# Kernel optimization log

Hardware: AMD Instinct MI355X
Metric: run time of the kernel (lower is better)

## Reference

```python
import jax, jax.numpy as jnp
import numpy as np

N = 400_000
B = 64          # number of segments (point clouds)
IN_C = 128
INTER = (256, 512, 512)
OUT_C = 512


def setup_inputs() -> dict:
    key = jax.random.key(0)
    ks = jax.random.split(key, 12)
    pos_emd = jax.random.normal(ks[0], (N, IN_C), dtype=jnp.float32)
    radius_p_batch = jnp.sort(jax.random.randint(ks[1], (N,), 0, B))

    def lin(k, fin, fout):
        kw, kb = jax.random.split(k)
        s = 1.0 / np.sqrt(fin)
        W = jax.random.uniform(kw, (fin, fout), jnp.float32, -s, s)
        b = jax.random.uniform(kb, (fout,), jnp.float32, -s, s)
        return W, b

    W1, b1 = lin(ks[2], IN_C, INTER[0])
    W2, b2 = lin(ks[3], INTER[0], INTER[1])
    W3, b3 = lin(ks[4], INTER[1], INTER[2])
    W4, b4 = lin(ks[5], IN_C + INTER[2], OUT_C)
    W5, b5 = lin(ks[6], OUT_C, OUT_C)
    return {
        "pos_emd": pos_emd, "radius_p_batch": radius_p_batch,
        "W1": W1, "b1": b1, "W2": W2, "b2": b2, "W3": W3, "b3": b3,
        "W4": W4, "b4": b4, "W5": W5, "b5": b5,
    }


def reference(pos_emd, radius_p_batch, W1, b1, W2, b2, W3, b3, W4, b4, W5, b5):
    # mlp1: Linear-ReLU-Linear-ReLU-Linear
    h = jax.nn.relu(pos_emd @ W1 + b1)
    h = jax.nn.relu(h @ W2 + b2)
    h = h @ W3 + b3                              # [N, 512]
    # global max pool over segments
    g = jax.ops.segment_max(h, radius_p_batch, num_segments=B)  # [B, 512]
    # broadcast each segment's global feature back to its points (ids sorted)
    g_rep = g[radius_p_batch]                    # [N, 512]
    z = jnp.concatenate((pos_emd, g_rep), axis=-1)  # [N, 640]
    # mlp2: Linear-ReLU-Linear
    z = jax.nn.relu(z @ W4 + b4)
    z = z @ W5 + b5                              # [N, 512]
    return jax.ops.segment_max(z, radius_p_batch, num_segments=B)  # [B, 512]
```

## Files before the change

### kernel.cpp

```cpp
#include <hip/hip_runtime.h>
#include <stdint.h>


typedef __bf16 bf16;
typedef __bf16 bf16x4 __attribute__((ext_vector_type(4)));
typedef __bf16 bf16x8 __attribute__((ext_vector_type(8)));
typedef float f32x4 __attribute__((ext_vector_type(4)));
typedef __attribute__((address_space(3))) char lds_char;

#define N_PTS 400000
#define ORD_NEG_INF 0x007FFFFFu

__device__ __forceinline__ unsigned f2ord(float f) {
  unsigned u = __float_as_uint(f);
  return (u & 0x80000000u) ? ~u : (u | 0x80000000u);
}
__device__ __forceinline__ float ord2f(unsigned o) {
  unsigned u = (o & 0x80000000u) ? (o ^ 0x80000000u) : ~o;
  return __uint_as_float(u);
}

__device__ __forceinline__ void gld16(const bf16* g, lds_char* l) {
  __builtin_amdgcn_global_load_lds((const __attribute__((address_space(1))) void*)g,
                                   (__attribute__((address_space(3))) void*)l, 16, 0, 0);
}

#define DSR(dst, preg, IMM) \
  asm volatile("ds_read_b128 %0, %1 offset:%c2" : "=&v"(dst) : "v"(preg), "n"(IMM))

#define SCHED0 __builtin_amdgcn_sched_barrier(0)
#define LGKM0 do { asm volatile("s_waitcnt lgkmcnt(0)"); SCHED0; } while (0)
#define SBARR do { __builtin_amdgcn_s_barrier(); SCHED0; } while (0)
#define VMW4 do { asm volatile("s_waitcnt vmcnt(4)"); SCHED0; } while (0)
#define VMW0 do { asm volatile("s_waitcnt vmcnt(0)"); SCHED0; } while (0)

__global__ void k_init(unsigned* g_ord, unsigned* out_u) {
  int i = blockIdx.x * 256 + threadIdx.x;
  if (i < 64 * 512) { g_ord[i] = ORD_NEG_INF; out_u[i] = ORD_NEG_INF; }
}

__global__ void k_convX(const float* __restrict__ x, bf16* __restrict__ y, long n4) {
  long i = (long)blockIdx.x * 256 + threadIdx.x;
  long stride = (long)gridDim.x * 256;
  for (; i < n4; i += stride) {
    float4 v = ((const float4*)x)[i];
    bf16x4 o = {(bf16)v.x, (bf16)v.y, (bf16)v.z, (bf16)v.w};
    ((bf16x4*)y)[i] = o;
  }
}

__global__ void k_convWt(const float* __restrict__ W, bf16* __restrict__ Wt, int K, int Nout) {
  int idx = blockIdx.x * 256 + threadIdx.x;
  if (idx < K * Nout) {
    int k = idx / Nout, c = idx - k * Nout;
    Wt[(size_t)c * K + k] = (bf16)W[idx];
  }
}

__global__ void k_segbias(const unsigned* __restrict__ g_ord, const float* __restrict__ W4,
                          const float* __restrict__ b4, float* __restrict__ sb) {
  const int s = blockIdx.x, c = threadIdx.x;
  __shared__ float gs[512];
  gs[c] = ord2f(g_ord[s * 512 + c]);
  __syncthreads();
  float acc = b4[c];
  for (int j = 0; j < 512; ++j) acc = fmaf(gs[j], W4[(size_t)(128 + j) * 512 + c], acc);
  sb[s * 512 + c] = acc;
}

__global__ void k_decode(unsigned* p, int n) {
  int i = blockIdx.x * 256 + threadIdx.x;
  if (i < n) { float f = ord2f(p[i]); ((float*)p)[i] = f; }
}

template <int BIASMODE, bool RELU, int EPI, int K, int NOUT>
__launch_bounds__(512, 1)
__global__ void k_gemm(const bf16* __restrict__ A, const bf16* __restrict__ Bt,
                       const float* __restrict__ bias, const int* __restrict__ ids,
                       long row_off, bf16* __restrict__ out,
                       unsigned* __restrict__ outAtomic) {
  constexpr int NT = K / 64;
  constexpr int NIT = NT / 2;
  constexpr int NBX = NOUT / 256;
  __shared__ __align__(16) char sMem[131072];
  __shared__ int sIds[256];
  const int tid = threadIdx.x;
  const int wid = tid >> 6, lane = tid & 63;
  const int wr = wid >> 2, wc = wid & 3;
  const int lr = lane & 15, lk = lane >> 4;

  const int nwg = NBX * (int)gridDim.y;
  const int orig = (int)blockIdx.y * NBX + (int)blockIdx.x;
  const int q = nwg >> 3, r = nwg & 7;
  const int xcd = orig & 7, lid = orig >> 3;
  const int wg = (xcd < r ? xcd * (q + 1) : r * (q + 1) + (xcd - r) * q) + lid;
  const int n0 = (wg % NBX) * 256;
  const int m0 = (wg / NBX) * 256;

  if constexpr (BIASMODE == 1 || EPI == 1) {
    if (tid < 256) {
      long gi = row_off + m0 + tid;
      if (gi > (long)N_PTS - 1) gi = (long)N_PTS - 1;
      sIds[tid] = ids[gi];
    }
  }
  SCHED0;

  const int row0 = (wid * 2) * 8 + (lane >> 3);
  const int row1 = row0 + 8;
  const int sc0 = ((lane & 7) ^ (lane >> 4)) * 8;
  const int sc1 = ((lane & 7) ^ (4 + (lane >> 4))) * 8;
  lds_char* lds3 = (lds_char*)sMem;

  auto stageH = [&](int tau, int mat, int h) {
    if (tau >= NT) return;
    const int db = tau & 1;
    const bf16* srcb = (mat == 0) ? A + (size_t)(m0 + h * 128) * K
                                  : Bt + (size_t)(n0 + h * 128) * K;
    lds_char* d0 = lds3 + mat * 65536 + h * 32768 + db * 16384 + (wid * 2) * 1024;
    gld16(srcb + (size_t)row0 * K + tau * 64 + sc0, d0);
    gld16(srcb + (size_t)row1 * K + tau * 64 + sc1, d0 + 1024);
  };

  const unsigned s7 = (unsigned)(lr >> 1);
  const unsigned cks0 = (((unsigned)lk) ^ s7) * 16u;
  const unsigned cks1 = (((unsigned)lk + 4u) ^ s7) * 16u;
  lds_char* vA0 = lds3 + wr * 32768 + lr * 128 + cks0;
  lds_char* vA1 = lds3 + wr * 32768 + lr * 128 + cks1;
  lds_char* vB0 = lds3 + 65536 + (wc >> 1) * 32768 + (wc & 1) * 8192 + lr * 128 + cks0;
  lds_char* vB1 = lds3 + 65536 + (wc >> 1) * 32768 + (wc & 1) * 8192 + lr * 128 + cks1;

  bf16x8 aR[4][2], bR[4][2];
  f32x4 acc[8][4];
#pragma unroll
  for (int i = 0; i < 8; ++i)
#pragma unroll
    for (int j = 0; j < 4; ++j) acc[i][j] = {0.f, 0.f, 0.f, 0.f};

#define RDA1(i, DB, IHI) \
  DSR(aR[i][0], vA0, (DB) + ((IHI) + (i)) * 2048); \
  DSR(aR[i][1], vA1, (DB) + ((IHI) + (i)) * 2048)
#define RD_A(DB, IHI) do { RDA1(0, DB, IHI); RDA1(1, DB, IHI); RDA1(2, DB, IHI); RDA1(3, DB, IHI); } while (0)
#define RDB1(j, DB) \
  DSR(bR[j][0], vB0, (DB) + (j) * 2048); \
  DSR(bR[j][1], vB1, (DB) + (j) * 2048)
#define RD_B01(DB) do { RDB1(0, DB); RDB1(1, DB); } while (0)
#define RD_B23(DB) do { RDB1(2, DB); RDB1(3, DB); } while (0)
#define MM(II, JJ) do { __builtin_amdgcn_s_setprio(1); \
  _Pragma("unroll") for (int i_ = 0; i_ < 4; ++i_) \
  _Pragma("unroll") for (int j_ = 0; j_ < 2; ++j_) { \
    acc[(II) + i_][(JJ) + j_] = __builtin_amdgcn_mfma_f32_16x16x32_bf16(aR[i_][0], bR[(JJ) + j_][0], acc[(II) + i_][(JJ) + j_], 0, 0, 0); \
    acc[(II) + i_][(JJ) + j_] = __builtin_amdgcn_mfma_f32_16x16x32_bf16(aR[i_][1], bR[(JJ) + j_][1], acc[(II) + i_][(JJ) + j_], 0, 0, 0); \
  } \
  __builtin_amdgcn_s_setprio(0); } while (0)

  stageH(0, 1, 0); stageH(0, 1, 1); stageH(0, 0, 0); stageH(0, 0, 1);
  stageH(1, 1, 0); stageH(1, 1, 1);
  asm volatile("s_waitcnt vmcnt(4) lgkmcnt(0)");
  SCHED0;
  SBARR;

#pragma unroll 1
  for (int t = 0; t < NIT; ++t) {
    const int t2 = 2 * t;
    RD_A(0, 0); RD_B01(0);
    stageH(t2 + 1, 0, 0);
    LGKM0; MM(0, 0); SBARR;
    RD_B23(0);
    stageH(t2 + 1, 0, 1);
    LGKM0; MM(0, 2); SBARR;
    RD_A(0, 4);
    stageH(t2 + 2, 1, 0);
    LGKM0; MM(4, 0); SBARR;
    stageH(t2 + 2, 1, 1);
    MM(4, 2);
    if (t < NIT - 1) VMW4; else VMW0;
    SBARR;
    RD_A(16384, 0); RD_B01(16384);
    stageH(t2 + 2, 0, 0);
    LGKM0; MM(0, 0); SBARR;
    RD_B23(16384);
    stageH(t2 + 2, 0, 1);
    LGKM0; MM(0, 2); SBARR;
    RD_A(16384, 4);
    stageH(t2 + 3, 1, 0);
    LGKM0; MM(4, 0); SBARR;
    stageH(t2 + 3, 1, 1);
    MM(4, 2);
    if (t < NIT - 1) { VMW4; SBARR; }
  }

  if constexpr (EPI == 0) {
#pragma unroll
    for (int j = 0; j < 4; ++j) {
      const int col = n0 + wc * 64 + j * 16 + lr;
      float bcol = (BIASMODE == 0) ? bias[col] : 0.f;
#pragma unroll
      for (int i = 0; i < 8; ++i) {
#pragma unroll
        for (int q2 = 0; q2 < 4; ++q2) {
          const int rl = wr * 128 + i * 16 + lk * 4 + q2;
          float v = acc[i][j][q2];
          if constexpr (BIASMODE == 0) v += bcol;
          else v += bias[(size_t)sIds[rl] * 512 + col];
          if constexpr (RELU) v = fmaxf(v, 0.f);
          out[(size_t)(m0 + rl) * NOUT + col] = (bf16)v;
        }
      }
    }
  } else {
    const int sLo = sIds[wr * 128], sHi = sIds[wr * 128 + 127];
#pragma unroll
    for (int j = 0; j < 4; ++j) {
      const int col = n0 + wc * 64 + j * 16 + lr;
      const float bcol = bias[col];
      for (int s = sLo; s <= sHi; ++s) {
        float m = -__builtin_inff();
#pragma unroll
        for (int i = 0; i < 8; ++i)
#pragma unroll
          for (int q2 = 0; q2 < 4; ++q2) {
            const int rl = wr * 128 + i * 16 + lk * 4 + q2;
            const bool rv = (row_off + m0 + rl) < (long)N_PTS;
            float v = acc[i][j][q2] + bcol;
            m = (sIds[rl] == s && rv) ? fmaxf(m, v) : m;
          }
        m = fmaxf(m, __shfl_xor(m, 16));
        m = fmaxf(m, __shfl_xor(m, 32));
        if (lane < 16) atomicMax(&outAtomic[(size_t)s * 512 + col], f2ord(m));
      }
    }
  }
#undef RDA1
#undef RD_A
#undef RDB1
#undef RD_B01
#undef RD_B23
#undef MM
}

static inline long lmin(long a, long b) { return a < b ? a : b; }

extern "C" void kernel_launch(void* const* d_in, const int* in_sizes, int n_in,
                              void* d_out, int out_size, void* d_ws, size_t ws_size,
                              hipStream_t stream) {
  const float* pos = (const float*)d_in[0];
  const int* ids = (const int*)d_in[1];
  const float* W1 = (const float*)d_in[2]; const float* b1 = (const float*)d_in[3];
  const float* W2 = (const float*)d_in[4]; const float* b2 = (const float*)d_in[5];
  const float* W3 = (const float*)d_in[6]; const float* b3 = (const float*)d_in[7];
  const float* W4 = (const float*)d_in[8]; const float* b4 = (const float*)d_in[9];
  const float* W5 = (const float*)d_in[10]; const float* b5 = (const float*)d_in[11];

  char* ws = (char*)d_ws;
  size_t off = 0;
  auto alloc = [&](size_t bytes) -> char* {
    off = (off + 255) & ~(size_t)255;
    char* p = ws + off; off += bytes; return p;
  };
  bf16* Wt1  = (bf16*)alloc(128 * 256 * 2);
  bf16* Wt2  = (bf16*)alloc(256 * 512 * 2);
  bf16* Wt3  = (bf16*)alloc(512 * 512 * 2);
  bf16* Wt4a = (bf16*)alloc(128 * 512 * 2);
  bf16* Wt5  = (bf16*)alloc(512 * 512 * 2);
  unsigned* g_ord = (unsigned*)alloc(64 * 512 * 4);
  float* sb = (float*)alloc(64 * 512 * 4);

  const size_t per_row = (128 + 256 + 512) * 2;
  size_t fixed_end = (off + 255) & ~(size_t)255;
  long avail = (long)ws_size - (long)fixed_end - 8192;
  long maxrows = avail / (long)per_row;
  long chunk = (maxrows - 256) & ~255L;
  if (chunk > N_PTS) chunk = N_PTS;
  if (chunk < 256) chunk = 256;
  long rows_alloc = chunk + 256;

  bf16* Xbf = (bf16*)alloc((size_t)rows_alloc * 128 * 2);
  bf16* h1  = (bf16*)alloc((size_t)rows_alloc * 256 * 2);
  bf16* h2  = (bf16*)alloc((size_t)rows_alloc * 512 * 2);

  const int nChunks = (int)((N_PTS + chunk - 1) / chunk);

  k_init<<<dim3(128), dim3(256), 0, stream>>>(g_ord, (unsigned*)d_out);
  k_convWt<<<dim3((128 * 256 + 255) / 256), dim3(256), 0, stream>>>(W1, Wt1, 128, 256);
  k_convWt<<<dim3((256 * 512 + 255) / 256), dim3(256), 0, stream>>>(W2, Wt2, 256, 512);
  k_convWt<<<dim3((512 * 512 + 255) / 256), dim3(256), 0, stream>>>(W3, Wt3, 512, 512);
  k_convWt<<<dim3((128 * 512 + 255) / 256), dim3(256), 0, stream>>>(W4, Wt4a, 128, 512);
  k_convWt<<<dim3((512 * 512 + 255) / 256), dim3(256), 0, stream>>>(W5, Wt5, 512, 512);

  for (long o = 0; o < N_PTS; o += chunk) {
    long rows = lmin(chunk, N_PTS - o);
    long n4 = rows * 32;
    long cb = lmin(2048, (n4 + 255) / 256);
    k_convX<<<dim3((unsigned)cb), dim3(256), 0, stream>>>(pos + o * 128, Xbf, n4);
    unsigned mb = (unsigned)((rows + 255) / 256);
    k_gemm<0, true, 0, 128, 256><<<dim3(1, mb), dim3(512), 0, stream>>>(Xbf, Wt1, b1, ids, o, h1, nullptr);
    k_gemm<0, true, 0, 256, 512><<<dim3(2, mb), dim3(512), 0, stream>>>(h1, Wt2, b2, ids, o, h2, nullptr);
    k_gemm<0, false, 1, 512, 512><<<dim3(2, mb), dim3(512), 0, stream>>>(h2, Wt3, b3, ids, o, nullptr, g_ord);
  }
  k_segbias<<<dim3(64), dim3(512), 0, stream>>>(g_ord, W4, b4, sb);
  for (long o = 0; o < N_PTS; o += chunk) {
    long rows = lmin(chunk, N_PTS - o);
    if (nChunks > 1) {
      long n4 = rows * 32;
      long cb = lmin(2048, (n4 + 255) / 256);
      k_convX<<<dim3((unsigned)cb), dim3(256), 0, stream>>>(pos + o * 128, Xbf, n4);
    }
    unsigned mb = (unsigned)((rows + 255) / 256);
    k_gemm<1, true, 0, 128, 512><<<dim3(2, mb), dim3(512), 0, stream>>>(Xbf, Wt4a, sb, ids, o, h2, nullptr);
    k_gemm<0, false, 1, 512, 512><<<dim3(2, mb), dim3(512), 0, stream>>>(h2, Wt5, b5, ids, o, nullptr, (unsigned*)d_out);
  }
  k_decode<<<dim3(128), dim3(256), 0, stream>>>((unsigned*)d_out, 64 * 512);
}
```

Before: 1.099 ms.

## Reschedule GEMM main loop with split A registers and hoist X conversion

The GEMM main loop is reordered so barriers come before the LDS reads wait, and A fragments use two register sets (aF/aS), letting the second-half A reads overlap the first-half MFMAs. Global-to-LDS staging is shifted by one stage, so the wait becomes vmcnt(2) instead of vmcnt(4). Separately, the bf16 conversion of the whole input is done once up front into a full-size buffer instead of per chunk, avoiding repeated conversion in the second pass when chunking occurs. The extra A registers raise register pressure, and the full-size X buffer shrinks the workspace left for chunks.

```diff
diff --git a/kernel.cpp b/kernel.cpp
--- a/kernel.cpp
+++ b/kernel.cpp
@@ -31,7 +31,7 @@
 #define SCHED0 __builtin_amdgcn_sched_barrier(0)
 #define LGKM0 do { asm volatile("s_waitcnt lgkmcnt(0)"); SCHED0; } while (0)
 #define SBARR do { __builtin_amdgcn_s_barrier(); SCHED0; } while (0)
-#define VMW4 do { asm volatile("s_waitcnt vmcnt(4)"); SCHED0; } while (0)
+#define VMW2 do { asm volatile("s_waitcnt vmcnt(2)"); SCHED0; } while (0)
 #define VMW0 do { asm volatile("s_waitcnt vmcnt(0)"); SCHED0; } while (0)
 
 __global__ void k_init(unsigned* g_ord, unsigned* out_u) {
@@ -130,64 +130,70 @@
   lds_char* vB0 = lds3 + 65536 + (wc >> 1) * 32768 + (wc & 1) * 8192 + lr * 128 + cks0;
   lds_char* vB1 = lds3 + 65536 + (wc >> 1) * 32768 + (wc & 1) * 8192 + lr * 128 + cks1;
 
-  bf16x8 aR[4][2], bR[4][2];
+  bf16x8 aF[4][2], aS[4][2], bR[4][2];
   f32x4 acc[8][4];
 #pragma unroll
   for (int i = 0; i < 8; ++i)
 #pragma unroll
     for (int j = 0; j < 4; ++j) acc[i][j] = {0.f, 0.f, 0.f, 0.f};
 
-#define RDA1(i, DB, IHI) \
-  DSR(aR[i][0], vA0, (DB) + ((IHI) + (i)) * 2048); \
-  DSR(aR[i][1], vA1, (DB) + ((IHI) + (i)) * 2048)
-#define RD_A(DB, IHI) do { RDA1(0, DB, IHI); RDA1(1, DB, IHI); RDA1(2, DB, IHI); RDA1(3, DB, IHI); } while (0)
+#define RDA4(ARR, DB, IHI) do { \
+  DSR(ARR[0][0], vA0, (DB) + ((IHI) + 0) * 2048); DSR(ARR[0][1], vA1, (DB) + ((IHI) + 0) * 2048); \
+  DSR(ARR[1][0], vA0, (DB) + ((IHI) + 1) * 2048); DSR(ARR[1][1], vA1, (DB) + ((IHI) + 1) * 2048); \
+  DSR(ARR[2][0], vA0, (DB) + ((IHI) + 2) * 2048); DSR(ARR[2][1], vA1, (DB) + ((IHI) + 2) * 2048); \
+  DSR(ARR[3][0], vA0, (DB) + ((IHI) + 3) * 2048); DSR(ARR[3][1], vA1, (DB) + ((IHI) + 3) * 2048); \
+} while (0)
 #define RDB1(j, DB) \
   DSR(bR[j][0], vB0, (DB) + (j) * 2048); \
   DSR(bR[j][1], vB1, (DB) + (j) * 2048)
 #define RD_B01(DB) do { RDB1(0, DB); RDB1(1, DB); } while (0)
 #define RD_B23(DB) do { RDB1(2, DB); RDB1(3, DB); } while (0)
-#define MM(II, JJ) do { __builtin_amdgcn_s_setprio(1); \
+#define MMQ(AARR, II, JJ) do { __builtin_amdgcn_s_setprio(1); \
   _Pragma("unroll") for (int i_ = 0; i_ < 4; ++i_) \
   _Pragma("unroll") for (int j_ = 0; j_ < 2; ++j_) { \
-    acc[(II) + i_][(JJ) + j_] = __builtin_amdgcn_mfma_f32_16x16x32_bf16(aR[i_][0], bR[(JJ) + j_][0], acc[(II) + i_][(JJ) + j_], 0, 0, 0); \
-    acc[(II) + i_][(JJ) + j_] = __builtin_amdgcn_mfma_f32_16x16x32_bf16(aR[i_][1], bR[(JJ) + j_][1], acc[(II) + i_][(JJ) + j_], 0, 0, 0); \
+    acc[(II) + i_][(JJ) + j_] = __builtin_amdgcn_mfma_f32_16x16x32_bf16(AARR[i_][0], bR[(JJ) + j_][0], acc[(II) + i_][(JJ) + j_], 0, 0, 0); \
+    acc[(II) + i_][(JJ) + j_] = __builtin_amdgcn_mfma_f32_16x16x32_bf16(AARR[i_][1], bR[(JJ) + j_][1], acc[(II) + i_][(JJ) + j_], 0, 0, 0); \
   } \
   __builtin_amdgcn_s_setprio(0); } while (0)
 
   stageH(0, 1, 0); stageH(0, 1, 1); stageH(0, 0, 0); stageH(0, 0, 1);
-  stageH(1, 1, 0); stageH(1, 1, 1);
-  asm volatile("s_waitcnt vmcnt(4) lgkmcnt(0)");
+  stageH(1, 1, 0);
+  asm volatile("s_waitcnt vmcnt(2) lgkmcnt(0)");
   SCHED0;
   SBARR;
 
 #pragma unroll 1
   for (int t = 0; t < NIT; ++t) {
     const int t2 = 2 * t;
-    RD_A(0, 0); RD_B01(0);
+    RDA4(aF, 0, 0); RD_B01(0);
+    stageH(t2 + 1, 1, 1);
+    SBARR; LGKM0; MMQ(aF, 0, 0);
+    RD_B23(0);
     stageH(t2 + 1, 0, 0);
-    LGKM0; MM(0, 0); SBARR;
-    RD_B23(0);
+    SBARR; LGKM0; MMQ(aF, 0, 2);
+    RDA4(aS, 0, 4);
     stageH(t2 + 1, 0, 1);
-    LGKM0; MM(0, 2); SBARR;
-    RD_A(0, 4);
+    SBARR; LGKM0; MMQ(aS, 4, 0);
     stageH(t2 + 2, 1, 0);
-    LGKM0; MM(4, 0); SBARR;
+    MMQ(aS, 4, 2);
+    if (t < NIT - 1) VMW2; else VMW0;
+    SBARR;
+    RDA4(aF, 16384, 0); RD_B01(16384);
     stageH(t2 + 2, 1, 1);
-    MM(4, 2);
-    if (t < NIT - 1) VMW4; else VMW0;
-    SBARR;
-    RD_A(16384, 0); RD_B01(16384);
+    SBARR; LGKM0; MMQ(aF, 0, 0);
+    RD_B23(16384);
     stageH(t2 + 2, 0, 0);
-    LGKM0; MM(0, 0); SBARR;
-    RD_B23(16384);
+    SBARR; LGKM0; MMQ(aF, 0, 2);
+    RDA4(aS, 16384, 4);
     stageH(t2 + 2, 0, 1);
-    LGKM0; MM(0, 2); SBARR;
-    RD_A(16384, 4);
-    stageH(t2 + 3, 1, 0);
-    LGKM0; MM(4, 0); SBARR;
-    stageH(t2 + 3, 1, 1);
-    MM(4, 2);
-    if (t < NIT - 1) { VMW4; SBARR; }
+    SBARR; LGKM0; MMQ(aS, 4, 0);
+    if (t < NIT - 1) {
+      stageH(t2 + 3, 1, 0);
+      MMQ(aS, 4, 2);
+      VMW2; SBARR;
+    } else {
+      MMQ(aS, 4, 2);
+    }
   }
 
   if constexpr (EPI == 0) {
@@ -231,12 +237,11 @@
       }
     }
   }
-#undef RDA1
-#undef RD_A
+#undef RDA4
 #undef RDB1
 #undef RD_B01
 #undef RD_B23
-#undef MM
+#undef MMQ
 }
 
 static inline long lmin(long a, long b) { return a < b ? a : b; }
@@ -265,8 +270,9 @@
   bf16* Wt5  = (bf16*)alloc(512 * 512 * 2);
   unsigned* g_ord = (unsigned*)alloc(64 * 512 * 4);
   float* sb = (float*)alloc(64 * 512 * 4);
-
-  const size_t per_row = (128 + 256 + 512) * 2;
+  bf16* Xbf = (bf16*)alloc((size_t)(N_PTS + 384) * 128 * 2);
+
+  const size_t per_row = (256 + 512) * 2;
   size_t fixed_end = (off + 255) & ~(size_t)255;
   long avail = (long)ws_size - (long)fixed_end - 8192;
   long maxrows = avail / (long)per_row;
@@ -275,11 +281,8 @@
   if (chunk < 256) chunk = 256;
   long rows_alloc = chunk + 256;
 
-  bf16* Xbf = (bf16*)alloc((size_t)rows_alloc * 128 * 2);
-  bf16* h1  = (bf16*)alloc((size_t)rows_alloc * 256 * 2);
-  bf16* h2  = (bf16*)alloc((size_t)rows_alloc * 512 * 2);
-
-  const int nChunks = (int)((N_PTS + chunk - 1) / chunk);
+  bf16* h1 = (bf16*)alloc((size_t)rows_alloc * 256 * 2);
+  bf16* h2 = (bf16*)alloc((size_t)rows_alloc * 512 * 2);
 
   k_init<<<dim3(128), dim3(256), 0, stream>>>(g_ord, (unsigned*)d_out);
   k_convWt<<<dim3((128 * 256 + 255) / 256), dim3(256), 0, stream>>>(W1, Wt1, 128, 256);
@@ -287,27 +290,20 @@
   k_convWt<<<dim3((512 * 512 + 255) / 256), dim3(256), 0, stream>>>(W3, Wt3, 512, 512);
   k_convWt<<<dim3((128 * 512 + 255) / 256), dim3(256), 0, stream>>>(W4, Wt4a, 128, 512);
   k_convWt<<<dim3((512 * 512 + 255) / 256), dim3(256), 0, stream>>>(W5, Wt5, 512, 512);
+  k_convX<<<dim3(2048), dim3(256), 0, stream>>>(pos, Xbf, (long)N_PTS * 32);
 
   for (long o = 0; o < N_PTS; o += chunk) {
     long rows = lmin(chunk, N_PTS - o);
-    long n4 = rows * 32;
-    long cb = lmin(2048, (n4 + 255) / 256);
-    k_convX<<<dim3((unsigned)cb), dim3(256), 0, stream>>>(pos + o * 128, Xbf, n4);
     unsigned mb = (unsigned)((rows + 255) / 256);
-    k_gemm<0, true, 0, 128, 256><<<dim3(1, mb), dim3(512), 0, stream>>>(Xbf, Wt1, b1, ids, o, h1, nullptr);
+    k_gemm<0, true, 0, 128, 256><<<dim3(1, mb), dim3(512), 0, stream>>>(Xbf + o * 128, Wt1, b1, ids, o, h1, nullptr);
     k_gemm<0, true, 0, 256, 512><<<dim3(2, mb), dim3(512), 0, stream>>>(h1, Wt2, b2, ids, o, h2, nullptr);
     k_gemm<0, false, 1, 512, 512><<<dim3(2, mb), dim3(512), 0, stream>>>(h2, Wt3, b3, ids, o, nullptr, g_ord);
   }
   k_segbias<<<dim3(64), dim3(512), 0, stream>>>(g_ord, W4, b4, sb);
   for (long o = 0; o < N_PTS; o += chunk) {
     long rows = lmin(chunk, N_PTS - o);
-    if (nChunks > 1) {
-      long n4 = rows * 32;
-      long cb = lmin(2048, (n4 + 255) / 256);
-      k_convX<<<dim3((unsigned)cb), dim3(256), 0, stream>>>(pos + o * 128, Xbf, n4);
-    }
     unsigned mb = (unsigned)((rows + 255) / 256);
-    k_gemm<1, true, 0, 128, 512><<<dim3(2, mb), dim3(512), 0, stream>>>(Xbf, Wt4a, sb, ids, o, h2, nullptr);
+    k_gemm<1, true, 0, 128, 512><<<dim3(2, mb), dim3(512), 0, stream>>>(Xbf + o * 128, Wt4a, sb, ids, o, h2, nullptr);
     k_gemm<0, false, 1, 512, 512><<<dim3(2, mb), dim3(512), 0, stream>>>(h2, Wt5, b5, ids, o, nullptr, (unsigned*)d_out);
   }
   k_decode<<<dim3(128), dim3(256), 0, stream>>>((unsigned*)d_out, 64 * 512);
```

After: 1.103 ms. No clear change (+0.3%).

## Make GEMM kernels persistent over M-tiles with a fixed grid and pipelined tile transitions

Applied to the files above, without the earlier changes.

Each GEMM kernel now launches a fixed grid of 256 CTAs (1 N-block) or 2x128 CTAs (2 N-blocks). Each CTA loops over several 256-row M-tiles, strided by the grid height. The K-loop staging runs continuously across tile boundaries, so the next tile's loads overlap the current tile's epilogue. This is meant to remove per-tile prologue/drain cost and wave-quantization tail effects. X is now converted to bf16 once for all rows instead of per chunk. The per-CTA id cache grows to 13 tiles, which bounds how many tiles one CTA can own. Extra A-register copies raise register pressure.

```diff
diff --git a/kernel.cpp b/kernel.cpp
--- a/kernel.cpp
+++ b/kernel.cpp
@@ -9,6 +9,8 @@
 typedef __attribute__((address_space(3))) char lds_char;
 
 #define N_PTS 400000
+#define MT_TOTAL ((N_PTS + 255) / 256)
+#define MAXMT 13
 #define ORD_NEG_INF 0x007FFFFFu
 
 __device__ __forceinline__ unsigned f2ord(float f) {
@@ -78,48 +80,56 @@
 __global__ void k_gemm(const bf16* __restrict__ A, const bf16* __restrict__ Bt,
                        const float* __restrict__ bias, const int* __restrict__ ids,
                        long row_off, bf16* __restrict__ out,
-                       unsigned* __restrict__ outAtomic) {
+                       unsigned* __restrict__ outAtomic, int MT) {
   constexpr int NT = K / 64;
+  constexpr int LOG2NT = (NT == 2 ? 1 : (NT == 4 ? 2 : 3));
   constexpr int NIT = NT / 2;
   constexpr int NBX = NOUT / 256;
   __shared__ __align__(16) char sMem[131072];
-  __shared__ int sIds[256];
+  __shared__ int sIdsAll[MAXMT][256];
   const int tid = threadIdx.x;
   const int wid = tid >> 6, lane = tid & 63;
   const int wr = wid >> 2, wc = wid & 3;
   const int lr = lane & 15, lk = lane >> 4;
 
-  const int nwg = NBX * (int)gridDim.y;
-  const int orig = (int)blockIdx.y * NBX + (int)blockIdx.x;
-  const int q = nwg >> 3, r = nwg & 7;
-  const int xcd = orig & 7, lid = orig >> 3;
-  const int wg = (xcd < r ? xcd * (q + 1) : r * (q + 1) + (xcd - r) * q) + lid;
-  const int n0 = (wg % NBX) * 256;
-  const int m0 = (wg / NBX) * 256;
+  const int n0 = (int)blockIdx.x * 256;
+  const int GY = (int)gridDim.y;
+  const int q = GY >> 3, r = GY & 7;
+  const int y = (int)blockIdx.y;
+  const int xcd = y & 7, lid = y >> 3;
+  const int swzY = (xcd < r ? xcd * (q + 1) : r * (q + 1) + (xcd - r) * q) + lid;
+  if (swzY >= MT) return;
+  const int myMT = (MT - 1 - swzY) / GY + 1;
+  const int totalT = myMT << LOG2NT;
+  const int totalIter = totalT >> 1;
 
   if constexpr (BIASMODE == 1 || EPI == 1) {
-    if (tid < 256) {
-      long gi = row_off + m0 + tid;
+    for (int m = (tid >> 8); m < myMT; m += 2) {
+      const int mt = swzY + m * GY;
+      long gi = row_off + (long)mt * 256 + (tid & 255);
       if (gi > (long)N_PTS - 1) gi = (long)N_PTS - 1;
-      sIds[tid] = ids[gi];
+      sIdsAll[m][tid & 255] = ids[gi];
     }
   }
   SCHED0;
 
-  const int row0 = (wid * 2) * 8 + (lane >> 3);
+  const int row0 = wid * 16 + (lane >> 3);
   const int row1 = row0 + 8;
   const int sc0 = ((lane & 7) ^ (lane >> 4)) * 8;
   const int sc1 = ((lane & 7) ^ (4 + (lane >> 4))) * 8;
   lds_char* lds3 = (lds_char*)sMem;
 
   auto stageH = [&](int tau, int mat, int h) {
-    if (tau >= NT) return;
+    if (tau >= totalT) return;
+    const int g = tau >> LOG2NT;
+    const int kt = tau & (NT - 1);
     const int db = tau & 1;
-    const bf16* srcb = (mat == 0) ? A + (size_t)(m0 + h * 128) * K
-                                  : Bt + (size_t)(n0 + h * 128) * K;
+    const bf16* srcb = (mat == 0)
+        ? A + (size_t)((swzY + g * GY) * 256 + h * 128) * K
+        : Bt + (size_t)(n0 + h * 128) * K;
     lds_char* d0 = lds3 + mat * 65536 + h * 32768 + db * 16384 + (wid * 2) * 1024;
-    gld16(srcb + (size_t)row0 * K + tau * 64 + sc0, d0);
-    gld16(srcb + (size_t)row1 * K + tau * 64 + sc1, d0 + 1024);
+    gld16(srcb + (size_t)row0 * K + kt * 64 + sc0, d0);
+    gld16(srcb + (size_t)row1 * K + kt * 64 + sc1, d0 + 1024);
   };
 
   const unsigned s7 = (unsigned)(lr >> 1);
@@ -130,27 +140,28 @@
   lds_char* vB0 = lds3 + 65536 + (wc >> 1) * 32768 + (wc & 1) * 8192 + lr * 128 + cks0;
   lds_char* vB1 = lds3 + 65536 + (wc >> 1) * 32768 + (wc & 1) * 8192 + lr * 128 + cks1;
 
-  bf16x8 aR[4][2], bR[4][2];
+  bf16x8 aR[4][2], aS[4][2], bR[4][2];
   f32x4 acc[8][4];
 #pragma unroll
   for (int i = 0; i < 8; ++i)
 #pragma unroll
     for (int j = 0; j < 4; ++j) acc[i][j] = {0.f, 0.f, 0.f, 0.f};
 
-#define RDA1(i, DB, IHI) \
-  DSR(aR[i][0], vA0, (DB) + ((IHI) + (i)) * 2048); \
-  DSR(aR[i][1], vA1, (DB) + ((IHI) + (i)) * 2048)
-#define RD_A(DB, IHI) do { RDA1(0, DB, IHI); RDA1(1, DB, IHI); RDA1(2, DB, IHI); RDA1(3, DB, IHI); } while (0)
+#define RDA1(ARR, i, DB, IHI) \
+  DSR(ARR[i][0], vA0, (DB) + ((IHI) + (i)) * 2048); \
+  DSR(ARR[i][1], vA1, (DB) + ((IHI) + (i)) * 2048)
+#define RD_A(ARR, DB, IHI) do { RDA1(ARR, 0, DB, IHI); RDA1(ARR, 1, DB, IHI); \
+                                RDA1(ARR, 2, DB, IHI); RDA1(ARR, 3, DB, IHI); } while (0)
 #define RDB1(j, DB) \
   DSR(bR[j][0], vB0, (DB) + (j) * 2048); \
   DSR(bR[j][1], vB1, (DB) + (j) * 2048)
 #define RD_B01(DB) do { RDB1(0, DB); RDB1(1, DB); } while (0)
 #define RD_B23(DB) do { RDB1(2, DB); RDB1(3, DB); } while (0)
-#define MM(II, JJ) do { __builtin_amdgcn_s_setprio(1); \
+#define MM(ARR, II, JJ) do { __builtin_amdgcn_s_setprio(1); \
   _Pragma("unroll") for (int i_ = 0; i_ < 4; ++i_) \
   _Pragma("unroll") for (int j_ = 0; j_ < 2; ++j_) { \
-    acc[(II) + i_][(JJ) + j_] = __builtin_amdgcn_mfma_f32_16x16x32_bf16(aR[i_][0], bR[(JJ) + j_][0], acc[(II) + i_][(JJ) + j_], 0, 0, 0); \
-    acc[(II) + i_][(JJ) + j_] = __builtin_amdgcn_mfma_f32_16x16x32_bf16(aR[i_][1], bR[(JJ) + j_][1], acc[(II) + i_][(JJ) + j_], 0, 0, 0); \
+    acc[(II) + i_][(JJ) + j_] = __builtin_amdgcn_mfma_f32_16x16x32_bf16(ARR[i_][0], bR[(JJ) + j_][0], acc[(II) + i_][(JJ) + j_], 0, 0, 0); \
+    acc[(II) + i_][(JJ) + j_] = __builtin_amdgcn_mfma_f32_16x16x32_bf16(ARR[i_][1], bR[(JJ) + j_][1], acc[(II) + i_][(JJ) + j_], 0, 0, 0); \
   } \
   __builtin_amdgcn_s_setprio(0); } while (0)
 
@@ -161,74 +172,83 @@
   SBARR;
 
 #pragma unroll 1
-  for (int t = 0; t < NIT; ++t) {
-    const int t2 = 2 * t;
-    RD_A(0, 0); RD_B01(0);
+  for (int it = 0; it < totalIter; ++it) {
+    const int t2 = 2 * it;
+    RD_A(aR, 0, 0); RD_B01(0);
     stageH(t2 + 1, 0, 0);
-    LGKM0; MM(0, 0); SBARR;
+    LGKM0; MM(aR, 0, 0); SBARR;
     RD_B23(0);
     stageH(t2 + 1, 0, 1);
-    LGKM0; MM(0, 2); SBARR;
-    RD_A(0, 4);
+    LGKM0; MM(aR, 0, 2); SBARR;
+    RD_A(aS, 0, 4);
     stageH(t2 + 2, 1, 0);
-    LGKM0; MM(4, 0); SBARR;
+    LGKM0; MM(aS, 4, 0); SBARR;
     stageH(t2 + 2, 1, 1);
-    MM(4, 2);
-    if (t < NIT - 1) VMW4; else VMW0;
+    MM(aS, 4, 2);
+    if (it < totalIter - 1) VMW4; else VMW0;
     SBARR;
-    RD_A(16384, 0); RD_B01(16384);
+    RD_A(aR, 16384, 0); RD_B01(16384);
     stageH(t2 + 2, 0, 0);
-    LGKM0; MM(0, 0); SBARR;
+    LGKM0; MM(aR, 0, 0); SBARR;
     RD_B23(16384);
     stageH(t2 + 2, 0, 1);
-    LGKM0; MM(0, 2); SBARR;
-    RD_A(16384, 4);
+    LGKM0; MM(aR, 0, 2); SBARR;
+    RD_A(aS, 16384, 4);
     stageH(t2 + 3, 1, 0);
-    LGKM0; MM(4, 0); SBARR;
+    LGKM0; MM(aS, 4, 0); SBARR;
     stageH(t2 + 3, 1, 1);
-    MM(4, 2);
-    if (t < NIT - 1) { VMW4; SBARR; }
-  }
-
-  if constexpr (EPI == 0) {
-#pragma unroll
-    for (int j = 0; j < 4; ++j) {
-      const int col = n0 + wc * 64 + j * 16 + lr;
-      float bcol = (BIASMODE == 0) ? bias[col] : 0.f;
-#pragma unroll
-      for (int i = 0; i < 8; ++i) {
-#pragma unroll
-        for (int q2 = 0; q2 < 4; ++q2) {
-          const int rl = wr * 128 + i * 16 + lk * 4 + q2;
-          float v = acc[i][j][q2];
-          if constexpr (BIASMODE == 0) v += bcol;
-          else v += bias[(size_t)sIds[rl] * 512 + col];
-          if constexpr (RELU) v = fmaxf(v, 0.f);
-          out[(size_t)(m0 + rl) * NOUT + col] = (bf16)v;
+    MM(aS, 4, 2);
+    if (it < totalIter - 1) { VMW4; SBARR; }
+
+    if (((it + 1) & (NIT - 1)) == 0) {
+      const int mloc = it >> (LOG2NT - 1);
+      const int m0 = (swzY + mloc * GY) * 256;
+      const int* sIds = &sIdsAll[mloc][0];
+      if constexpr (EPI == 0) {
+#pragma unroll
+        for (int j = 0; j < 4; ++j) {
+          const int col = n0 + wc * 64 + j * 16 + lr;
+          float bcol = (BIASMODE == 0) ? bias[col] : 0.f;
+#pragma unroll
+          for (int i = 0; i < 8; ++i) {
+#pragma unroll
+            for (int q2 = 0; q2 < 4; ++q2) {
+              const int rl = wr * 128 + i * 16 + lk * 4 + q2;
+              float v = acc[i][j][q2];
+              if constexpr (BIASMODE == 0) v += bcol;
+              else v += bias[(size_t)sIds[rl] * 512 + col];
+              if constexpr (RELU) v = fmaxf(v, 0.f);
+              out[(size_t)(m0 + rl) * NOUT + col] = (bf16)v;
+            }
+          }
+        }
+      } else {
+        const int sLo = sIds[wr * 128], sHi = sIds[wr * 128 + 127];
+#pragma unroll
+        for (int j = 0; j < 4; ++j) {
+          const int col = n0 + wc * 64 + j * 16 + lr;
+          const float bcol = bias[col];
+          for (int s = sLo; s <= sHi; ++s) {
+            float m = -__builtin_inff();
+#pragma unroll
+            for (int i = 0; i < 8; ++i)
+#pragma unroll
+              for (int q2 = 0; q2 < 4; ++q2) {
+                const int rl = wr * 128 + i * 16 + lk * 4 + q2;
+                const bool rv = (row_off + m0 + rl) < (long)N_PTS;
+                float v = acc[i][j][q2] + bcol;
+                m = (sIds[rl] == s && rv) ? fmaxf(m, v) : m;
+              }
+            m = fmaxf(m, __shfl_xor(m, 16));
+            m = fmaxf(m, __shfl_xor(m, 32));
+            if (lane < 16) atomicMax(&outAtomic[(size_t)s * 512 + col], f2ord(m));
+          }
         }
       }
-    }
-  } else {
-    const int sLo = sIds[wr * 128], sHi = sIds[wr * 128 + 127];
-#pragma unroll
-    for (int j = 0; j < 4; ++j) {
-      const int col = n0 + wc * 64 + j * 16 + lr;
-      const float bcol = bias[col];
-      for (int s = sLo; s <= sHi; ++s) {
-        float m = -__builtin_inff();
-#pragma unroll
-        for (int i = 0; i < 8; ++i)
-#pragma unroll
-          for (int q2 = 0; q2 < 4; ++q2) {
-            const int rl = wr * 128 + i * 16 + lk * 4 + q2;
-            const bool rv = (row_off + m0 + rl) < (long)N_PTS;
-            float v = acc[i][j][q2] + bcol;
-            m = (sIds[rl] == s && rv) ? fmaxf(m, v) : m;
-          }
-        m = fmaxf(m, __shfl_xor(m, 16));
-        m = fmaxf(m, __shfl_xor(m, 32));
-        if (lane < 16) atomicMax(&outAtomic[(size_t)s * 512 + col], f2ord(m));
-      }
+#pragma unroll
+      for (int i = 0; i < 8; ++i)
+#pragma unroll
+        for (int j = 0; j < 4; ++j) acc[i][j] = {0.f, 0.f, 0.f, 0.f};
     }
   }
 #undef RDA1
@@ -265,21 +285,18 @@
   bf16* Wt5  = (bf16*)alloc(512 * 512 * 2);
   unsigned* g_ord = (unsigned*)alloc(64 * 512 * 4);
   float* sb = (float*)alloc(64 * 512 * 4);
-
-  const size_t per_row = (128 + 256 + 512) * 2;
+  bf16* Xbf = (bf16*)alloc((size_t)(MT_TOTAL * 256) * 128 * 2);
+
+  const size_t per_row = (256 + 512) * 2;
   size_t fixed_end = (off + 255) & ~(size_t)255;
   long avail = (long)ws_size - (long)fixed_end - 8192;
-  long maxrows = avail / (long)per_row;
-  long chunk = (maxrows - 256) & ~255L;
-  if (chunk > N_PTS) chunk = N_PTS;
-  if (chunk < 256) chunk = 256;
-  long rows_alloc = chunk + 256;
-
-  bf16* Xbf = (bf16*)alloc((size_t)rows_alloc * 128 * 2);
-  bf16* h1  = (bf16*)alloc((size_t)rows_alloc * 256 * 2);
-  bf16* h2  = (bf16*)alloc((size_t)rows_alloc * 512 * 2);
-
-  const int nChunks = (int)((N_PTS + chunk - 1) / chunk);
+  long maxrows = (avail / (long)per_row) & ~255L;
+  long chRows = lmin(maxrows, (long)MT_TOTAL * 256);
+  if (chRows < 256) chRows = 256;
+  const int chMT = (int)(chRows / 256);
+
+  bf16* h1 = (bf16*)alloc((size_t)chRows * 256 * 2);
+  bf16* h2 = (bf16*)alloc((size_t)chRows * 512 * 2);
 
   k_init<<<dim3(128), dim3(256), 0, stream>>>(g_ord, (unsigned*)d_out);
   k_convWt<<<dim3((128 * 256 + 255) / 256), dim3(256), 0, stream>>>(W1, Wt1, 128, 256);
@@ -287,28 +304,26 @@
   k_convWt<<<dim3((512 * 512 + 255) / 256), dim3(256), 0, stream>>>(W3, Wt3, 512, 512);
   k_convWt<<<dim3((128 * 512 + 255) / 256), dim3(256), 0, stream>>>(W4, Wt4a, 128, 512);
   k_convWt<<<dim3((512 * 512 + 255) / 256), dim3(256), 0, stream>>>(W5, Wt5, 512, 512);
-
-  for (long o = 0; o < N_PTS; o += chunk) {
-    long rows = lmin(chunk, N_PTS - o);
-    long n4 = rows * 32;
-    long cb = lmin(2048, (n4 + 255) / 256);
-    k_convX<<<dim3((unsigned)cb), dim3(256), 0, stream>>>(pos + o * 128, Xbf, n4);
-    unsigned mb = (unsigned)((rows + 255) / 256);
-    k_gemm<0, true, 0, 128, 256><<<dim3(1, mb), dim3(512), 0, stream>>>(Xbf, Wt1, b1, ids, o, h1, nullptr);
-    k_gemm<0, true, 0, 256, 512><<<dim3(2, mb), dim3(512), 0, stream>>>(h1, Wt2, b2, ids, o, h2, nullptr);
-    k_gemm<0, false, 1, 512, 512><<<dim3(2, mb), dim3(512), 0, stream>>>(h2, Wt3, b3, ids, o, nullptr, g_ord);
+  k_convX<<<dim3(2048), dim3(256), 0, stream>>>(pos, Xbf, (long)N_PTS * 32);
+
+  for (int mtOff = 0; mtOff < MT_TOTAL; mtOff += chMT) {
+    const int thisMT = (int)lmin(chMT, MT_TOTAL - mtOff);
+    const long ro = (long)mtOff * 256;
+    k_gemm<0, true, 0, 128, 256><<<dim3(1, 256), dim3(512), 0, stream>>>(
+        Xbf + ro * 128, Wt1, b1, ids, ro, h1, nullptr, thisMT);
+    k_gemm<0, true, 0, 256, 512><<<dim3(2, 128), dim3(512), 0, stream>>>(
+        h1, Wt2, b2, ids, ro, h2, nullptr, thisMT);
+    k_gemm<0, false, 1, 512, 512><<<dim3(2, 128), dim3(512), 0, stream>>>(
+        h2, Wt3, b3, ids, ro, nullptr, g_ord, thisMT);
   }
   k_segbias<<<dim3(64), dim3(512), 0, stream>>>(g_ord, W4, b4, sb);
-  for (long o = 0; o < N_PTS; o += chunk) {
-    long rows = lmin(chunk, N_PTS - o);
-    if (nChunks > 1) {
-      long n4 = rows * 32;
-      long cb = lmin(2048, (n4 + 255) / 256);
-      k_convX<<<dim3((unsigned)cb), dim3(256), 0, stream>>>(pos + o * 128, Xbf, n4);
-    }
-    unsigned mb = (unsigned)((rows + 255) / 256);
-    k_gemm<1, true, 0, 128, 512><<<dim3(2, mb), dim3(512), 0, stream>>>(Xbf, Wt4a, sb, ids, o, h2, nullptr);
-    k_gemm<0, false, 1, 512, 512><<<dim3(2, mb), dim3(512), 0, stream>>>(h2, Wt5, b5, ids, o, nullptr, (unsigned*)d_out);
+  for (int mtOff = 0; mtOff < MT_TOTAL; mtOff += chMT) {
+    const int thisMT = (int)lmin(chMT, MT_TOTAL - mtOff);
+    const long ro = (long)mtOff * 256;
+    k_gemm<1, true, 0, 128, 512><<<dim3(2, 128), dim3(512), 0, stream>>>(
+        Xbf + ro * 128, Wt4a, sb, ids, ro, h2, nullptr, thisMT);
+    k_gemm<0, false, 1, 512, 512><<<dim3(2, 128), dim3(512), 0, stream>>>(
+        h2, Wt5, b5, ids, ro, nullptr, (unsigned*)d_out, thisMT);
   }
   k_decode<<<dim3(128), dim3(256), 0, stream>>>((unsigned*)d_out, 64 * 512);
 }
```

Result: slower. 1.229 ms (+11.8%).
